# Performance work log

Measured on AMD Instinct MI355X. Metric: run time of the kernel, lower is better.

The kernel has to match this reference:

```python
import jax, jax.numpy as jnp
import numpy as np


def setup_inputs() -> dict:
    key = jax.random.key(0)
    k1, k2 = jax.random.split(key)
    B, T, N = 4, 8, 2048
    pred = jax.random.normal(k1, (B, T, N), dtype=jnp.float32)
    target = jax.random.normal(k2, (B, T, N), dtype=jnp.float32)
    return {"pred": pred, "target": target}


def reference(pred, target):
    # Kendall-tau loss: sort target by pred order, count concordant/discordant pairs.
    pred = pred.astype(jnp.float32)
    target = target.astype(jnp.float32)
    idx = jnp.argsort(pred, axis=2)                      # [B,T,N]
    target_a = jnp.take_along_axis(target, idx, axis=2)  # [B,T,N]
    B, T, N = target_a.shape
    M = N - 1
    refs = target_a[:, :, :-1, None]                     # [B,T,M,1] (row i = i-th element)
    ex = target_a[:, :, None, :]                         # [B,T,1,N] (col j = j-th element)
    mask = jnp.triu(jnp.ones((M, N), dtype=bool), k=1)   # pairs with j > i
    greater = (ex > refs) & mask                         # [B,T,M,N]
    lesser = (ex < refs) & mask
    conc = jnp.sum(greater, axis=(-1, -2))[..., None].astype(jnp.float32)  # [B,T,1]
    disc = jnp.sum(lesser, axis=(-1, -2))[..., None].astype(jnp.float32)
    tau = (conc - disc) / (conc + disc)
    loss = 1.0 - tau
    return loss.mean()
```

## Files before the change

kernel.cpp:

```cpp
#include <hip/hip_runtime.h>

#define NN 2048
#define ROWS 32
#define TS 128
#define NT (NN / TS)
#define NPAIR (NT * (NT + 1) / 2)
#define GRID (ROWS * NPAIR)
#define THREADS 64

typedef float v2f __attribute__((ext_vector_type(2)));

__global__ __launch_bounds__(THREADS) void ktau_count(const float* __restrict__ pred,
                                                      const float* __restrict__ target,
                                                      int* __restrict__ ws) {
    __shared__ v2f jtile[TS];

    const int blk = blockIdx.x;
    const int row = blk / NPAIR;
    int t = blk - row * NPAIR;
    int ta = 0, base = 0;
    while (t >= base + (NT - ta)) { base += NT - ta; ++ta; }
    const int tb = ta + (t - base);

    const float* __restrict__ prow = pred   + row * NN;
    const float* __restrict__ qrow = target + row * NN;
    const int tid = threadIdx.x;

    #pragma unroll
    for (int t2 = tid; t2 < TS; t2 += THREADS) {
        int j = tb * TS + t2;
        v2f v; v.x = prow[j]; v.y = qrow[j];
        jtile[t2] = v;
    }

    const int i0 = ta * TS + tid * 2;
    float2 pp = *(const float2*)(prow + i0);
    float2 qq = *(const float2*)(qrow + i0);
    v2f pq0; pq0.x = pp.x; pq0.y = qq.x;
    v2f pq1; pq1.x = pp.y; pq1.y = qq.y;
    __syncthreads();

    unsigned disc = 0;
    for (int h = 0; h < TS / 32; ++h) {
        unsigned b0 = 0, b1 = 0;
        #pragma unroll
        for (int jj = 0; jj < 32; ++jj) {
            v2f pqj = jtile[h * 32 + jj];
            v2f d0 = pqj - pq0;
            v2f d1 = pqj - pq1;
            unsigned x0 = (unsigned)(__float_as_int(d0.x) ^ __float_as_int(d0.y));
            unsigned x1 = (unsigned)(__float_as_int(d1.x) ^ __float_as_int(d1.y));
            b0 = __builtin_amdgcn_alignbit(b0, x0, 31);
            b1 = __builtin_amdgcn_alignbit(b1, x1, 31);
        }
        disc += __builtin_popcount(b0) + __builtin_popcount(b1);
    }

    int d = (int)disc;
    #pragma unroll
    for (int off = 32; off > 0; off >>= 1)
        d += __shfl_down(d, off, 64);
    if (tid == 0)
        ws[blk] = (ta == tb) ? d : (d << 1);
}

__global__ __launch_bounds__(256) void ktau_final(const int* __restrict__ ws,
                                                  float* __restrict__ out) {
    __shared__ int wpart[4];
    const int tid = threadIdx.x;
    int v = 0;
    for (int b = tid; b < GRID; b += 256) v += ws[b];
    #pragma unroll
    for (int off = 32; off > 0; off >>= 1)
        v += __shfl_down(v, off, 64);
    if ((tid & 63) == 0) wpart[tid >> 6] = v;
    __syncthreads();
    if (tid == 0) {
        const float invT = 1.0f / (float)(((long long)NN * (NN - 1)) / 2);
        int total = wpart[0] + wpart[1] + wpart[2] + wpart[3];
        out[0] = (float)total * invT / (float)ROWS;
    }
}

extern "C" void kernel_launch(void* const* d_in, const int* in_sizes, int n_in,
                              void* d_out, int out_size, void* d_ws, size_t ws_size,
                              hipStream_t stream) {
    const float* pred   = (const float*)d_in[0];
    const float* target = (const float*)d_in[1];
    float* out = (float*)d_out;
    int* ws    = (int*)d_ws;

    ktau_count<<<GRID, THREADS, 0, stream>>>(pred, target, ws);
    ktau_final<<<1, 256, 0, stream>>>(ws, out);
}
```

Before: 67.92 us.

## Count discordant pairs with wave ballots and scalar popcount instead of per-lane bitpacking

Replaces per-lane sign-XOR and alignbit bit packing with wave-wide ballots of comparisons, XOR-ed and popcounted on scalar registers. This makes the count wave-uniform and removes the final shuffle reduction. The shared tile becomes a float4 pair layout loaded with one vectorized store per thread. The intent is fewer VALU ops per pair by moving the counting onto the scalar unit, at the cost of a serial dependence on SALU ballot results and a slight change in tie semantics.

Result: no change. 67.44 us (-0.7%).

```diff
diff --git a/kernel.cpp b/kernel.cpp
--- a/kernel.cpp
+++ b/kernel.cpp
@@ -8,12 +8,12 @@
 #define GRID (ROWS * NPAIR)
 #define THREADS 64
 
-typedef float v2f __attribute__((ext_vector_type(2)));
+typedef float v4f __attribute__((ext_vector_type(4)));
 
 __global__ __launch_bounds__(THREADS) void ktau_count(const float* __restrict__ pred,
                                                       const float* __restrict__ target,
                                                       int* __restrict__ ws) {
-    __shared__ v2f jtile[TS];
+    __shared__ v4f jtile[TS / 2];
 
     const int blk = blockIdx.x;
     const int row = blk / NPAIR;
@@ -26,42 +26,36 @@
     const float* __restrict__ qrow = target + row * NN;
     const int tid = threadIdx.x;
 
-    #pragma unroll
-    for (int t2 = tid; t2 < TS; t2 += THREADS) {
-        int j = tb * TS + t2;
-        v2f v; v.x = prow[j]; v.y = qrow[j];
-        jtile[t2] = v;
+    {
+        const int j0 = tb * TS + tid * 2;
+        float2 pj = *(const float2*)(prow + j0);
+        float2 qj = *(const float2*)(qrow + j0);
+        v4f v; v.x = pj.x; v.y = qj.x; v.z = pj.y; v.w = qj.y;
+        jtile[tid] = v;
     }
 
     const int i0 = ta * TS + tid * 2;
     float2 pp = *(const float2*)(prow + i0);
     float2 qq = *(const float2*)(qrow + i0);
-    v2f pq0; pq0.x = pp.x; pq0.y = qq.x;
-    v2f pq1; pq1.x = pp.y; pq1.y = qq.y;
     __syncthreads();
 
     unsigned disc = 0;
-    for (int h = 0; h < TS / 32; ++h) {
-        unsigned b0 = 0, b1 = 0;
-        #pragma unroll
-        for (int jj = 0; jj < 32; ++jj) {
-            v2f pqj = jtile[h * 32 + jj];
-            v2f d0 = pqj - pq0;
-            v2f d1 = pqj - pq1;
-            unsigned x0 = (unsigned)(__float_as_int(d0.x) ^ __float_as_int(d0.y));
-            unsigned x1 = (unsigned)(__float_as_int(d1.x) ^ __float_as_int(d1.y));
-            b0 = __builtin_amdgcn_alignbit(b0, x0, 31);
-            b1 = __builtin_amdgcn_alignbit(b1, x1, 31);
-        }
-        disc += __builtin_popcount(b0) + __builtin_popcount(b1);
+    #pragma unroll 8
+    for (int jj = 0; jj < TS / 2; ++jj) {
+        v4f j2 = jtile[jj];
+        unsigned long long a, b;
+        a = __ballot(j2.x > pp.x); b = __ballot(j2.y > qq.x);
+        disc += (unsigned)__popcll(a ^ b);
+        a = __ballot(j2.x > pp.y); b = __ballot(j2.y > qq.y);
+        disc += (unsigned)__popcll(a ^ b);
+        a = __ballot(j2.z > pp.x); b = __ballot(j2.w > qq.x);
+        disc += (unsigned)__popcll(a ^ b);
+        a = __ballot(j2.z > pp.y); b = __ballot(j2.w > qq.y);
+        disc += (unsigned)__popcll(a ^ b);
     }
 
-    int d = (int)disc;
-    #pragma unroll
-    for (int off = 32; off > 0; off >>= 1)
-        d += __shfl_down(d, off, 64);
     if (tid == 0)
-        ws[blk] = (ta == tb) ? d : (d << 1);
+        ws[blk] = (ta == tb) ? (int)disc : (int)(disc << 1);
 }
 
 __global__ __launch_bounds__(256) void ktau_final(const int* __restrict__ ws,
```
